# Kernel optimization log

Measured on AMD Instinct MI355X. Metric: run time of the kernel, lower is better.

Reference implementation:

```python
import jax, jax.numpy as jnp
import numpy as np

HEADS, DH, RS = 8, 32, 16  # heads, dim_head, reduce_size

def _dwconv(x, w):
    # depthwise 3x3, pad=1, stride=1 (OIHW with I=1, groups=C)
    return jax.lax.conv_general_dilated(x, w, (1, 1), [(1, 1), (1, 1)],
        dimension_numbers=('NCHW', 'OIHW', 'NCHW'), feature_group_count=x.shape[1])

def _pwconv(x, w):
    return jax.lax.conv_general_dilated(x, w, (1, 1), 'VALID',
        dimension_numbers=('NCHW', 'OIHW', 'NCHW'))

def _bilinear_ac(x, oh, ow):
    # F.interpolate(mode='bilinear', align_corners=True)
    B, C, H, W = x.shape
    ys = jnp.linspace(0., H - 1., oh)
    xs = jnp.linspace(0., W - 1., ow)
    y0 = jnp.floor(ys).astype(jnp.int32); y1 = jnp.minimum(y0 + 1, H - 1)
    x0 = jnp.floor(xs).astype(jnp.int32); x1 = jnp.minimum(x0 + 1, W - 1)
    wy = (ys - y0)[None, None, :, None]
    wx = (xs - x0)[None, None, None, :]
    top = x[:, :, y0, :] * (1. - wy) + x[:, :, y1, :] * wy
    return top[:, :, :, x0] * (1. - wx) + top[:, :, :, x1] * wx

def _ln(t, g, b, eps=1e-6):
    # per-head LayerNorm over last dim; g,b: [heads, dim_head]
    mu = t.mean(-1, keepdims=True)
    var = ((t - mu) ** 2).mean(-1, keepdims=True)
    return (t - mu) / jnp.sqrt(var + eps) * g[None, :, None, :] + b[None, :, None, :]

def setup_inputs() -> dict:
    key = jax.random.key(0)
    ks = jax.random.split(key, 6)
    C = HEADS * DH  # 256
    x = jax.random.normal(ks[0], (8, C, 64, 64), jnp.float32)
    qkv_dw = jax.random.normal(ks[1], (C, 1, 3, 3), jnp.float32) * 0.05
    qkv_pw = jax.random.normal(ks[2], (3 * C, C, 1, 1), jnp.float32) * 0.05
    out_dw = jax.random.normal(ks[3], (C, 1, 3, 3), jnp.float32) * 0.05
    out_pw = jax.random.normal(ks[4], (C, C, 1, 1), jnp.float32) * 0.05
    gq = jnp.ones((HEADS, DH), jnp.float32); bq = jnp.zeros((HEADS, DH), jnp.float32)
    gk = jnp.ones((HEADS, DH), jnp.float32); bk = jnp.zeros((HEADS, DH), jnp.float32)
    bias_table = jax.random.normal(ks[5], ((2 * RS - 1) * (2 * RS - 1), HEADS), jnp.float32) * 0.02
    # relative_position_index buffer, exactly as in RelativePositionBias.__init__
    coords = np.stack(np.meshgrid(np.arange(RS), np.arange(RS), indexing='ij')).reshape(2, -1)
    rel = (coords[:, :, None] - coords[:, None, :]).transpose(1, 2, 0).copy()
    rel[:, :, 0] += RS - 1; rel[:, :, 1] += RS - 1; rel[:, :, 0] *= 2 * RS - 1
    rel_index = jnp.asarray(rel.sum(-1), jnp.int32)  # [RS*RS, RS*RS]
    return dict(x=x, qkv_dw=qkv_dw, qkv_pw=qkv_pw, out_dw=out_dw, out_pw=out_pw,
                gq=gq, bq=bq, gk=gk, bk=bk, bias_table=bias_table, rel_index=rel_index)

def reference(x, qkv_dw, qkv_pw, out_dw, out_pw, gq, bq, gk, bk, bias_table, rel_index):
    B, C, H, W = x.shape
    qkv = _pwconv(_dwconv(x, qkv_dw), qkv_pw)          # [B, 3*inner_dim, H, W]
    q, k, v = jnp.split(qkv, 3, axis=1)
    k = _bilinear_ac(k, RS, RS)
    v = _bilinear_ac(v, RS, RS)
    def heads(t):  # 'b (dim_head heads) h w -> b heads (h w) dim_head'
        b, _, hh, ww = t.shape
        return t.reshape(b, DH, HEADS, hh * ww).transpose(0, 2, 3, 1)
    q = _ln(heads(q), gq, bq)                           # [B, h, H*W, DH]
    k = _ln(heads(k), gk, bk)                           # [B, h, RS*RS, DH]
    v = heads(v)
    attn = jnp.einsum('bhid,bhjd->bhij', q, k)          # [B, h, H*W, RS*RS]
    # relative position bias: gather + repeat_interleave expansion
    bias = bias_table[rel_index.reshape(-1)].reshape(RS, RS, RS * RS, HEADS)
    bias = jnp.repeat(jnp.repeat(bias, H // RS, axis=0), W // RS, axis=1)
    bias = bias.reshape(H * W, RS * RS, HEADS).transpose(2, 0, 1)[None]
    attn = (attn + bias) * (1.0 / DH)                   # scale = dim_head ** -1 (no softmax)
    out = jnp.einsum('bhij,bhjd->bhid', attn, v)        # [B, h, H*W, DH]
    out = out.reshape(B, HEADS, H, W, DH).transpose(0, 4, 1, 2, 3).reshape(B, DH * HEADS, H, W)
    out = _pwconv(_dwconv(out, out_dw), out_pw)
    return out, attn
```

## Files before the change

### kernel.cpp

```cpp
#include <hip/hip_runtime.h>
#include <cstdint>

#define HW_ 4096

typedef __attribute__((ext_vector_type(8))) short bf16x8;
typedef __attribute__((ext_vector_type(4))) short bf16x4;
typedef __attribute__((ext_vector_type(4))) float f32x4;

static __device__ __forceinline__ unsigned short f2bf(float f) {
  unsigned u = __builtin_bit_cast(unsigned, f);
  u += 0x7FFF + ((u >> 16) & 1);
  return (unsigned short)(u >> 16);
}
static __device__ __forceinline__ float bf2f(unsigned short u) {
  return __builtin_bit_cast(float, (unsigned)u << 16);
}
static __device__ __forceinline__ float ldf(const float* p) { return *p; }
static __device__ __forceinline__ float ldf(const unsigned short* p) { return bf2f(*p); }

static __device__ __forceinline__ void gl_lds16(const unsigned short* g,
                                                unsigned short* s) {
  __builtin_amdgcn_global_load_lds(
      (const __attribute__((address_space(1))) unsigned int*)g,
      (__attribute__((address_space(3))) unsigned int*)s, 16, 0, 0);
}

template <typename T, int DO_PREP>
__global__ __launch_bounds__(256) void dwconv_t_kernel(
    const T* __restrict__ x, const float* __restrict__ w9,
    unsigned short* __restrict__ xT,
    const float* __restrict__ pw1, const float* __restrict__ pw2,
    unsigned short* __restrict__ wb, const float* __restrict__ btab,
    const int* __restrict__ relidx, float* __restrict__ bias_pre) {
  if (DO_PREP && blockIdx.z == 8) {
    int idx0 = (blockIdx.y * 64 + blockIdx.x) * 256 + threadIdx.x;
#pragma unroll
    for (int k = 0; k < 12; ++k) {
      int idx = idx0 + k * 65536;
      if (idx < 262144) {
        wb[idx] = f2bf(idx < 196608 ? pw1[idx] : pw2[idx - 196608]);
      } else {
        int t = idx - 262144;
        int j = t & 255, g = (t >> 8) & 255, h = t >> 16;
        bias_pre[t] = btab[relidx[g * 256 + j] * 8 + h] * 0.03125f;
      }
    }
    return;
  }
  __shared__ unsigned short lds_t[64][66];
  int iy = blockIdx.x;
  int cg = blockIdx.y;
  int b  = blockIdx.z;
  int tid = threadIdx.x;
  int px  = tid & 63;
  int cl0 = (tid >> 6) * 16;
  const T* xrow = x + (size_t)b * 256 * HW_ + iy * 64 + px;
#pragma unroll 4
  for (int e = 0; e < 16; ++e) {
    int c = cg * 64 + cl0 + e;
    const T* xp = xrow + (size_t)c * HW_;
    const float* wp = w9 + c * 9;
    float v0 = (iy > 0)  ? ldf(xp - 64) : 0.f;
    float v1 = ldf(xp);
    float v2 = (iy < 63) ? ldf(xp + 64) : 0.f;
    float l0 = __shfl(v0, px - 1, 64), r0 = __shfl(v0, px + 1, 64);
    float l1 = __shfl(v1, px - 1, 64), r1 = __shfl(v1, px + 1, 64);
    float l2 = __shfl(v2, px - 1, 64), r2 = __shfl(v2, px + 1, 64);
    if (px == 0)  { l0 = 0.f; l1 = 0.f; l2 = 0.f; }
    if (px == 63) { r0 = 0.f; r1 = 0.f; r2 = 0.f; }
    float acc = l0 * wp[0] + v0 * wp[1] + r0 * wp[2]
              + l1 * wp[3] + v1 * wp[4] + r1 * wp[5]
              + l2 * wp[6] + v2 * wp[7] + r2 * wp[8];
    lds_t[cl0 + e][px] = f2bf(acc);
  }
  __syncthreads();
#pragma unroll
  for (int j = 0; j < 2; ++j) {
    int flat = tid + j * 256;
    int rpx = flat >> 3, cseg = flat & 7;
    unsigned v0 = (unsigned)lds_t[cseg*8+0][rpx] | ((unsigned)lds_t[cseg*8+1][rpx] << 16);
    unsigned v1 = (unsigned)lds_t[cseg*8+2][rpx] | ((unsigned)lds_t[cseg*8+3][rpx] << 16);
    unsigned v2 = (unsigned)lds_t[cseg*8+4][rpx] | ((unsigned)lds_t[cseg*8+5][rpx] << 16);
    unsigned v3 = (unsigned)lds_t[cseg*8+6][rpx] | ((unsigned)lds_t[cseg*8+7][rpx] << 16);
    uint4 pk = {v0, v1, v2, v3};
    *(uint4*)(xT + ((size_t)b * 4096 + iy * 64 + rpx) * 256 + cg * 64 + cseg * 8) = pk;
  }
}

template <int OUT_BF16, int KV>
__global__ __launch_bounds__(256) void pwconv_mfma_kernel(
    const unsigned short* __restrict__ XT, const unsigned short* __restrict__ W,
    void* __restrict__ Yv, int OC,
    const float* __restrict__ gk, const float* __restrict__ bk,
    unsigned short* __restrict__ kln, unsigned short* __restrict__ vfrag) {
  __shared__ unsigned short As[128 * 64];
  __shared__ unsigned short Bs[128 * 64];
  int tid = threadIdx.x;
  int b = blockIdx.z;
  if (KV && blockIdx.y == 2) {
    float (*xds)[260] = (float(*)[260])As;
    int j0 = blockIdx.x * 8;
    {
      int pt = tid >> 5, icg = tid & 31;
      int j = j0 + pt;
      int oy = j >> 4, ox = j & 15;
      const float s = 63.0f / 15.0f;
      float ys = oy * s, xf = ox * s;
      int y0 = (int)ys, x0 = (int)xf;
      int y1 = min(y0 + 1, 63), x1 = min(x0 + 1, 63);
      float wy = ys - (float)y0, wx = xf - (float)x0;
      float w00 = (1.f - wy) * (1.f - wx), w01 = (1.f - wy) * wx;
      float w10 = wy * (1.f - wx), w11 = wy * wx;
      const unsigned short* base = XT + (size_t)b * 4096 * 256 + icg * 8;
      bf16x8 a00 = *(const bf16x8*)(base + (size_t)(y0 * 64 + x0) * 256);
      bf16x8 a01 = *(const bf16x8*)(base + (size_t)(y0 * 64 + x1) * 256);
      bf16x8 a10 = *(const bf16x8*)(base + (size_t)(y1 * 64 + x0) * 256);
      bf16x8 a11 = *(const bf16x8*)(base + (size_t)(y1 * 64 + x1) * 256);
#pragma unroll
      for (int e = 0; e < 8; ++e) {
        xds[pt][icg * 8 + e] =
            w00 * bf2f((unsigned short)a00[e]) + w01 * bf2f((unsigned short)a01[e]) +
            w10 * bf2f((unsigned short)a10[e]) + w11 * bf2f((unsigned short)a11[e]);
      }
    }
    __syncthreads();
    int pt = tid & 7, grp = tid >> 3;
    int isv = grp >> 4, h = (grp >> 1) & 7, dh = grp & 1;
    int j = j0 + pt;
    int bh = b * 8 + h;
    float acc[16] = {};
    const unsigned short* Wb = W + (size_t)(256 + isv * 256 + dh * 128 + h) * 256;
    for (int c8 = 0; c8 < 32; ++c8) {
      const float4* xr = (const float4*)&xds[pt][c8 * 8];
      float4 xa = xr[0], xb = xr[1];
#pragma unroll
      for (int dd = 0; dd < 16; ++dd) {
        bf16x8 wv = *(const bf16x8*)(Wb + (size_t)dd * 8 * 256 + c8 * 8);
        acc[dd] += bf2f((unsigned short)wv[0]) * xa.x + bf2f((unsigned short)wv[1]) * xa.y
                 + bf2f((unsigned short)wv[2]) * xa.z + bf2f((unsigned short)wv[3]) * xa.w
                 + bf2f((unsigned short)wv[4]) * xb.x + bf2f((unsigned short)wv[5]) * xb.y
                 + bf2f((unsigned short)wv[6]) * xb.z + bf2f((unsigned short)wv[7]) * xb.w;
      }
    }
    if (isv == 0) {
      float s1 = 0.f, s2 = 0.f;
#pragma unroll
      for (int dd = 0; dd < 16; ++dd) { s1 += acc[dd]; s2 += acc[dd] * acc[dd]; }
      s1 += __shfl_xor(s1, 8, 64);
      s2 += __shfl_xor(s2, 8, 64);
      float mu = s1 * (1.f / 32.f);
      float var = s2 * (1.f / 32.f) - mu * mu;
      float inv = 1.0f / sqrtf(var + 1e-6f);
      unsigned r[8];
#pragma unroll
      for (int t = 0; t < 8; ++t) {
        int d = dh * 16 + 2 * t;
        float y0f = (acc[2*t]   - mu) * inv * gk[h*32 + d]     + bk[h*32 + d];
        float y1f = (acc[2*t+1] - mu) * inv * gk[h*32 + d + 1] + bk[h*32 + d + 1];
        r[t] = (unsigned)f2bf(y0f) | ((unsigned)f2bf(y1f) << 16);
      }
      unsigned short* ko = kln + ((size_t)bh * 256 + j) * 32 + dh * 16;
      uint4 p0 = {r[0], r[1], r[2], r[3]};
      uint4 p1 = {r[4], r[5], r[6], r[7]};
      *(uint4*)ko = p0;
      *(uint4*)(ko + 8) = p1;
    } else {
      int c = j >> 4, gq2 = (j >> 2) & 3, ii = j & 3;
      unsigned short* vo = vfrag + (size_t)bh * 32 * 256 + (c * 2 + dh) * 256 + ii;
#pragma unroll
      for (int dd = 0; dd < 16; ++dd)
        vo[(gq2 * 16 + dd) * 4] = f2bf(acc[dd]);
    }
    return;
  }
  int oc0 = blockIdx.y * 128, p0 = blockIdx.x * 128;
  int w = tid >> 6, l = tid & 63;
  int wm = w >> 1, wn = w & 1;
  int lr = l & 15, lg = l >> 4;
  const unsigned short* Wp = W + (size_t)oc0 * 256;
  const unsigned short* Xp = XT + ((size_t)b * 4096 + p0) * 256;
  f32x4 acc[4][4] = {};
  for (int kt = 0; kt < 4; ++kt) {
    int k0 = kt * 64;
#pragma unroll
    for (int j = 0; j < 4; ++j) {
      int chunk = w * 4 + j;
      int row = chunk * 8 + (l >> 3);
      int lcu = (l & 7) ^ (row & 7);
      gl_lds16(Wp + (size_t)row * 256 + k0 + lcu * 8, &As[chunk * 512]);
      gl_lds16(Xp + (size_t)row * 256 + k0 + lcu * 8, &Bs[chunk * 512]);
    }
    __syncthreads();
#pragma unroll
    for (int ks = 0; ks < 2; ++ks) {
      bf16x8 af[4], bfr[4];
      int ku = ks * 4 + lg;
#pragma unroll
      for (int mi = 0; mi < 4; ++mi) {
        int row = wm * 64 + mi * 16 + lr;
        af[mi] = *(const bf16x8*)&As[row * 64 + (ku ^ (row & 7)) * 8];
      }
#pragma unroll
      for (int ni = 0; ni < 4; ++ni) {
        int row = wn * 64 + ni * 16 + lr;
        bfr[ni] = *(const bf16x8*)&Bs[row * 64 + (ku ^ (row & 7)) * 8];
      }
#pragma unroll
      for (int mi = 0; mi < 4; ++mi)
#pragma unroll
        for (int ni = 0; ni < 4; ++ni)
          acc[mi][ni] = __builtin_amdgcn_mfma_f32_16x16x32_bf16(
              af[mi], bfr[ni], acc[mi][ni], 0, 0, 0);
    }
    __syncthreads();
  }
  if constexpr (OUT_BF16) {
    __shared__ unsigned short Cs[128][136];
#pragma unroll
    for (int mi = 0; mi < 4; ++mi)
#pragma unroll
      for (int ni = 0; ni < 4; ++ni)
#pragma unroll
        for (int r = 0; r < 4; ++r)
          Cs[wm * 64 + mi * 16 + lg * 4 + r][wn * 64 + ni * 16 + lr] =
              f2bf(acc[mi][ni][r]);
    __syncthreads();
    unsigned short* Yb = (unsigned short*)Yv + (size_t)b * OC * HW_;
    int pc = tid & 15, ocr = tid >> 4;
#pragma unroll
    for (int it = 0; it < 8; ++it) {
      int oc = it * 16 + ocr;
      uint4 pk = *(const uint4*)&Cs[oc][pc * 8];
      *(uint4*)(Yb + (size_t)(oc0 + oc) * HW_ + p0 + pc * 8) = pk;
    }
  } else {
    float* Yb = (float*)Yv + (size_t)b * OC * HW_;
#pragma unroll
    for (int mi = 0; mi < 4; ++mi)
#pragma unroll
      for (int ni = 0; ni < 4; ++ni)
#pragma unroll
        for (int r = 0; r < 4; ++r) {
          int oc = oc0 + wm * 64 + mi * 16 + lg * 4 + r;
          int p  = p0 + wn * 64 + ni * 16 + lr;
          Yb[(size_t)oc * HW_ + p] = acc[mi][ni][r];
        }
  }
}

__global__ __launch_bounds__(256) void attn_mfma_kernel(
    const unsigned short* __restrict__ qb, const float* __restrict__ gq,
    const float* __restrict__ bq, const unsigned short* __restrict__ kln,
    const unsigned short* __restrict__ vfrag, const float* __restrict__ bias_pre,
    float* __restrict__ attn_out, unsigned short* __restrict__ out_nchw) {
  int tile = blockIdx.x, h = blockIdx.y, b = blockIdx.z;
  int bh = b * 8 + h;
  int tid = threadIdx.x;
  int w = tid >> 6, l = tid & 63;
  int lr = l & 15, lg = l >> 4;
  int qbase = tile * 64 + w * 16;
  int q = qbase + lr;
  int iy = q >> 6, ix = q & 63;
  int g = (iy >> 2) * 16 + (ix >> 2);

  const unsigned short* qp = qb + ((size_t)b * 256 + h) * HW_ + q;
  float qv[8];
  float sum = 0.f, sum2 = 0.f;
#pragma unroll
  for (int e = 0; e < 8; ++e) {
    qv[e] = bf2f(qp[(size_t)((lg * 8 + e) * 8) * HW_]);
    sum += qv[e]; sum2 += qv[e] * qv[e];
  }
  sum  += __shfl_xor(sum, 16, 64);  sum  += __shfl_xor(sum, 32, 64);
  sum2 += __shfl_xor(sum2, 16, 64); sum2 += __shfl_xor(sum2, 32, 64);
  float mu = sum * (1.f / 32.f);
  float var = sum2 * (1.f / 32.f) - mu * mu;
  float inv = 1.0f / sqrtf(var + 1e-6f);
  bf16x8 qf;
#pragma unroll
  for (int e = 0; e < 8; ++e) {
    int d = lg * 8 + e;
    float y = (qv[e] - mu) * inv * gq[h * 32 + d] + bq[h * 32 + d];
    qf[e] = (short)f2bf(y);
  }

  const unsigned short* kbase = kln + (size_t)bh * 256 * 32 + lr * 32 + lg * 8;
  const unsigned short* vbase = vfrag + (size_t)bh * 32 * 256 + l * 4;
  const float* bbase = bias_pre + ((size_t)h * 256 + g) * 256 + lg * 4;
  float* abase = attn_out + ((size_t)bh * 4096 + q) * 256 + lg * 4;

  f32x4 z = {0.f, 0.f, 0.f, 0.f};
  f32x4 oacc0 = z, oacc1 = z;
#pragma unroll
  for (int c = 0; c < 16; ++c) {
    bf16x8 kf = *(const bf16x8*)(kbase + c * 16 * 32);
    f32x4 s = __builtin_amdgcn_mfma_f32_16x16x32_bf16(kf, qf, z, 0, 0, 0);
    f32x4 bias = *(const f32x4*)(bbase + c * 16);
    f32x4 t = s * 0.03125f + bias;
    __builtin_nontemporal_store(t, (f32x4*)(abase + c * 16));
    bf16x4 pb;
    pb[0] = (short)f2bf(t.x);
    pb[1] = (short)f2bf(t.y);
    pb[2] = (short)f2bf(t.z);
    pb[3] = (short)f2bf(t.w);
    bf16x4 va0 = *(const bf16x4*)(vbase + (c * 2 + 0) * 256);
    bf16x4 va1 = *(const bf16x4*)(vbase + (c * 2 + 1) * 256);
    oacc0 = __builtin_amdgcn_mfma_f32_16x16x16bf16_1k(va0, pb, oacc0, 0, 0, 0);
    oacc1 = __builtin_amdgcn_mfma_f32_16x16x16bf16_1k(va1, pb, oacc1, 0, 0, 0);
  }
  float ov[8] = {oacc0.x, oacc0.y, oacc0.z, oacc0.w,
                 oacc1.x, oacc1.y, oacc1.z, oacc1.w};
#pragma unroll
  for (int dt = 0; dt < 2; ++dt) {
#pragma unroll
    for (int r = 0; r < 4; ++r) {
      int d = dt * 16 + lg * 4 + r;
      int cc = d * 8 + h;
      out_nchw[((size_t)b * 256 + cc) * HW_ + qbase + lr] = f2bf(ov[dt * 4 + r]);
    }
  }
}

extern "C" void kernel_launch(void* const* d_in, const int* in_sizes, int n_in,
                              void* d_out, int out_size, void* d_ws, size_t ws_size,
                              hipStream_t stream) {
  const float* x      = (const float*)d_in[0];
  const float* qkv_dw = (const float*)d_in[1];
  const float* qkv_pw = (const float*)d_in[2];
  const float* out_dw = (const float*)d_in[3];
  const float* out_pw = (const float*)d_in[4];
  const float* gq     = (const float*)d_in[5];
  const float* bq     = (const float*)d_in[6];
  const float* gk     = (const float*)d_in[7];
  const float* bk     = (const float*)d_in[8];
  const float* btab   = (const float*)d_in[9];
  const int*   relidx = (const int*)d_in[10];

  float* out  = (float*)d_out;
  float* attn = out + 8388608;

  unsigned short* us = (unsigned short*)d_ws;
  unsigned short* xT1    = us;
  unsigned short* xT2    = us + 8388608;
  unsigned short* onchwb = us + 16777216;
  unsigned short* kln    = us + 25165824;
  unsigned short* vfrag  = us + 25690112;
  unsigned short* wbuf   = us + 26214400;
  float* bias_pre = (float*)(us + 26476544);
  unsigned short* qb     = us + 27525120;

  dwconv_t_kernel<float, 1><<<dim3(64, 4, 9), 256, 0, stream>>>(
      x, qkv_dw, xT1, qkv_pw, out_pw, wbuf, btab, relidx, bias_pre);
  pwconv_mfma_kernel<1, 1><<<dim3(32, 3, 8), 256, 0, stream>>>(
      xT1, wbuf, qb, 256, gk, bk, kln, vfrag);
  attn_mfma_kernel<<<dim3(64, 8, 8), 256, 0, stream>>>(qb, gq, bq, kln, vfrag,
                                                       bias_pre, attn, onchwb);
  dwconv_t_kernel<unsigned short, 0><<<dim3(64, 4, 8), 256, 0, stream>>>(
      onchwb, out_dw, xT2, nullptr, nullptr, nullptr, nullptr, nullptr, nullptr);
  pwconv_mfma_kernel<0, 0><<<dim3(32, 2, 8), 256, 0, stream>>>(
      xT2, wbuf + 196608, out, 256, nullptr, nullptr, nullptr, nullptr);
}
```

Before: 168.6 us.

## Move K/V projection to separate MFMA GEMM kernel with head-permuted weights

The scalar FP32 K/V projection that ran inside the q pwconv kernel is replaced. That kernel now only bilinearly downsamples the input to a bf16 buffer. A new kv_gemm_kernel then does the K/V projection with bf16 MFMA, followed by LayerNorm and the vfrag scatter. The weight prep permutes the K/V weight rows so that each head's channels are contiguous, and the LDS is shared with the epilogue buffer. This trades an extra kernel launch, a global round-trip of the downsampled tensor, and bf16 rounding of the downsampled input for much cheaper matrix math.

```diff
diff --git a/kernel.cpp b/kernel.cpp
--- a/kernel.cpp
+++ b/kernel.cpp
@@ -37,8 +37,20 @@
 #pragma unroll
     for (int k = 0; k < 12; ++k) {
       int idx = idx0 + k * 65536;
-      if (idx < 262144) {
-        wb[idx] = f2bf(idx < 196608 ? pw1[idx] : pw2[idx - 196608]);
+      if (idx < 65536) {
+        wb[idx] = f2bf(pw1[idx]);
+      } else if (idx < 131072) {
+        int t = idx - 65536;
+        int row = t >> 8, col = t & 255;
+        int h = row >> 5, d = row & 31;
+        wb[idx] = f2bf(pw1[(256 + d * 8 + h) * 256 + col]);
+      } else if (idx < 196608) {
+        int t = idx - 131072;
+        int row = t >> 8, col = t & 255;
+        int h = row >> 5, d = row & 31;
+        wb[idx] = f2bf(pw1[(512 + d * 8 + h) * 256 + col]);
+      } else if (idx < 262144) {
+        wb[idx] = f2bf(pw2[idx - 196608]);
       } else {
         int t = idx - 262144;
         int j = t & 255, g = (t >> 8) & 255, h = t >> 16;
@@ -90,86 +102,45 @@
 template <int OUT_BF16, int KV>
 __global__ __launch_bounds__(256) void pwconv_mfma_kernel(
     const unsigned short* __restrict__ XT, const unsigned short* __restrict__ W,
-    void* __restrict__ Yv, int OC,
-    const float* __restrict__ gk, const float* __restrict__ bk,
-    unsigned short* __restrict__ kln, unsigned short* __restrict__ vfrag) {
-  __shared__ unsigned short As[128 * 64];
-  __shared__ unsigned short Bs[128 * 64];
+    void* __restrict__ Yv, int OC, unsigned short* __restrict__ xds) {
+  __shared__ unsigned short smem[18432];
+  unsigned short* As = smem;
+  unsigned short* Bs = smem + 8192;
   int tid = threadIdx.x;
   int b = blockIdx.z;
   if (KV && blockIdx.y == 2) {
-    float (*xds)[260] = (float(*)[260])As;
-    int j0 = blockIdx.x * 8;
-    {
-      int pt = tid >> 5, icg = tid & 31;
-      int j = j0 + pt;
-      int oy = j >> 4, ox = j & 15;
-      const float s = 63.0f / 15.0f;
-      float ys = oy * s, xf = ox * s;
-      int y0 = (int)ys, x0 = (int)xf;
-      int y1 = min(y0 + 1, 63), x1 = min(x0 + 1, 63);
-      float wy = ys - (float)y0, wx = xf - (float)x0;
-      float w00 = (1.f - wy) * (1.f - wx), w01 = (1.f - wy) * wx;
-      float w10 = wy * (1.f - wx), w11 = wy * wx;
-      const unsigned short* base = XT + (size_t)b * 4096 * 256 + icg * 8;
-      bf16x8 a00 = *(const bf16x8*)(base + (size_t)(y0 * 64 + x0) * 256);
-      bf16x8 a01 = *(const bf16x8*)(base + (size_t)(y0 * 64 + x1) * 256);
-      bf16x8 a10 = *(const bf16x8*)(base + (size_t)(y1 * 64 + x0) * 256);
-      bf16x8 a11 = *(const bf16x8*)(base + (size_t)(y1 * 64 + x1) * 256);
-#pragma unroll
-      for (int e = 0; e < 8; ++e) {
-        xds[pt][icg * 8 + e] =
-            w00 * bf2f((unsigned short)a00[e]) + w01 * bf2f((unsigned short)a01[e]) +
-            w10 * bf2f((unsigned short)a10[e]) + w11 * bf2f((unsigned short)a11[e]);
-      }
-    }
-    __syncthreads();
-    int pt = tid & 7, grp = tid >> 3;
-    int isv = grp >> 4, h = (grp >> 1) & 7, dh = grp & 1;
-    int j = j0 + pt;
-    int bh = b * 8 + h;
-    float acc[16] = {};
-    const unsigned short* Wb = W + (size_t)(256 + isv * 256 + dh * 128 + h) * 256;
-    for (int c8 = 0; c8 < 32; ++c8) {
-      const float4* xr = (const float4*)&xds[pt][c8 * 8];
-      float4 xa = xr[0], xb = xr[1];
-#pragma unroll
-      for (int dd = 0; dd < 16; ++dd) {
-        bf16x8 wv = *(const bf16x8*)(Wb + (size_t)dd * 8 * 256 + c8 * 8);
-        acc[dd] += bf2f((unsigned short)wv[0]) * xa.x + bf2f((unsigned short)wv[1]) * xa.y
-                 + bf2f((unsigned short)wv[2]) * xa.z + bf2f((unsigned short)wv[3]) * xa.w
-                 + bf2f((unsigned short)wv[4]) * xb.x + bf2f((unsigned short)wv[5]) * xb.y
-                 + bf2f((unsigned short)wv[6]) * xb.z + bf2f((unsigned short)wv[7]) * xb.w;
-      }
-    }
-    if (isv == 0) {
-      float s1 = 0.f, s2 = 0.f;
-#pragma unroll
-      for (int dd = 0; dd < 16; ++dd) { s1 += acc[dd]; s2 += acc[dd] * acc[dd]; }
-      s1 += __shfl_xor(s1, 8, 64);
-      s2 += __shfl_xor(s2, 8, 64);
-      float mu = s1 * (1.f / 32.f);
-      float var = s2 * (1.f / 32.f) - mu * mu;
-      float inv = 1.0f / sqrtf(var + 1e-6f);
-      unsigned r[8];
-#pragma unroll
-      for (int t = 0; t < 8; ++t) {
-        int d = dh * 16 + 2 * t;
-        float y0f = (acc[2*t]   - mu) * inv * gk[h*32 + d]     + bk[h*32 + d];
-        float y1f = (acc[2*t+1] - mu) * inv * gk[h*32 + d + 1] + bk[h*32 + d + 1];
-        r[t] = (unsigned)f2bf(y0f) | ((unsigned)f2bf(y1f) << 16);
-      }
-      unsigned short* ko = kln + ((size_t)bh * 256 + j) * 32 + dh * 16;
-      uint4 p0 = {r[0], r[1], r[2], r[3]};
-      uint4 p1 = {r[4], r[5], r[6], r[7]};
-      *(uint4*)ko = p0;
-      *(uint4*)(ko + 8) = p1;
-    } else {
-      int c = j >> 4, gq2 = (j >> 2) & 3, ii = j & 3;
-      unsigned short* vo = vfrag + (size_t)bh * 32 * 256 + (c * 2 + dh) * 256 + ii;
-#pragma unroll
-      for (int dd = 0; dd < 16; ++dd)
-        vo[(gq2 * 16 + dd) * 4] = f2bf(acc[dd]);
+    if (blockIdx.x >= 8) return;
+    int j0 = blockIdx.x * 32;
+    int jloc = tid >> 3, icg = tid & 7;
+    int j = j0 + jloc;
+    int oy = j >> 4, ox = j & 15;
+    const float s = 63.0f / 15.0f;
+    float ys = oy * s, xf = ox * s;
+    int y0 = (int)ys, x0 = (int)xf;
+    int y1 = min(y0 + 1, 63), x1 = min(x0 + 1, 63);
+    float wy = ys - (float)y0, wx = xf - (float)x0;
+    float w00 = (1.f - wy) * (1.f - wx), w01 = (1.f - wy) * wx;
+    float w10 = wy * (1.f - wx), w11 = wy * wx;
+    const unsigned short* base = XT + (size_t)b * 4096 * 256 + icg * 32;
+    const bf16x8* p00 = (const bf16x8*)(base + (size_t)(y0 * 64 + x0) * 256);
+    const bf16x8* p01 = (const bf16x8*)(base + (size_t)(y0 * 64 + x1) * 256);
+    const bf16x8* p10 = (const bf16x8*)(base + (size_t)(y1 * 64 + x0) * 256);
+    const bf16x8* p11 = (const bf16x8*)(base + (size_t)(y1 * 64 + x1) * 256);
+    unsigned short* xo = xds + ((size_t)(b * 256 + j)) * 256 + icg * 32;
+#pragma unroll
+    for (int q = 0; q < 4; ++q) {
+      bf16x8 a00 = p00[q], a01 = p01[q], a10 = p10[q], a11 = p11[q];
+      unsigned rp[4];
+#pragma unroll
+      for (int e2 = 0; e2 < 4; ++e2) {
+        float f0 = w00 * bf2f((unsigned short)a00[2*e2])   + w01 * bf2f((unsigned short)a01[2*e2])
+                 + w10 * bf2f((unsigned short)a10[2*e2])   + w11 * bf2f((unsigned short)a11[2*e2]);
+        float f1 = w00 * bf2f((unsigned short)a00[2*e2+1]) + w01 * bf2f((unsigned short)a01[2*e2+1])
+                 + w10 * bf2f((unsigned short)a10[2*e2+1]) + w11 * bf2f((unsigned short)a11[2*e2+1]);
+        rp[e2] = (unsigned)f2bf(f0) | ((unsigned)f2bf(f1) << 16);
+      }
+      uint4 pk = {rp[0], rp[1], rp[2], rp[3]};
+      *(uint4*)(xo + q * 8) = pk;
     }
     return;
   }
@@ -215,7 +186,7 @@
     __syncthreads();
   }
   if constexpr (OUT_BF16) {
-    __shared__ unsigned short Cs[128][136];
+    unsigned short (*Cs)[136] = (unsigned short(*)[136])smem;
 #pragma unroll
     for (int mi = 0; mi < 4; ++mi)
 #pragma unroll
@@ -245,6 +216,117 @@
           int p  = p0 + wn * 64 + ni * 16 + lr;
           Yb[(size_t)oc * HW_ + p] = acc[mi][ni][r];
         }
+  }
+}
+
+__global__ __launch_bounds__(256) void kv_gemm_kernel(
+    const unsigned short* __restrict__ XDS, const unsigned short* __restrict__ W,
+    const float* __restrict__ gk, const float* __restrict__ bk,
+    unsigned short* __restrict__ kln, unsigned short* __restrict__ vfrag) {
+  __shared__ unsigned short smem[18432];
+  unsigned short* As = smem;
+  unsigned short* Bs = smem + 8192;
+  int tid = threadIdx.x;
+  int b = blockIdx.z, yv = blockIdx.y;
+  int oc0 = yv * 128, p0 = blockIdx.x * 128;
+  int w = tid >> 6, l = tid & 63;
+  int wm = w >> 1, wn = w & 1;
+  int lr = l & 15, lg = l >> 4;
+  const unsigned short* Wp = W + (size_t)oc0 * 256;
+  const unsigned short* Xp = XDS + ((size_t)b * 256 + p0) * 256;
+  f32x4 acc[4][4] = {};
+  for (int kt = 0; kt < 4; ++kt) {
+    int k0 = kt * 64;
+#pragma unroll
+    for (int j = 0; j < 4; ++j) {
+      int chunk = w * 4 + j;
+      int row = chunk * 8 + (l >> 3);
+      int lcu = (l & 7) ^ (row & 7);
+      gl_lds16(Wp + (size_t)row * 256 + k0 + lcu * 8, &As[chunk * 512]);
+      gl_lds16(Xp + (size_t)row * 256 + k0 + lcu * 8, &Bs[chunk * 512]);
+    }
+    __syncthreads();
+#pragma unroll
+    for (int ks = 0; ks < 2; ++ks) {
+      bf16x8 af[4], bfr[4];
+      int ku = ks * 4 + lg;
+#pragma unroll
+      for (int mi = 0; mi < 4; ++mi) {
+        int row = wm * 64 + mi * 16 + lr;
+        af[mi] = *(const bf16x8*)&As[row * 64 + (ku ^ (row & 7)) * 8];
+      }
+#pragma unroll
+      for (int ni = 0; ni < 4; ++ni) {
+        int row = wn * 64 + ni * 16 + lr;
+        bfr[ni] = *(const bf16x8*)&Bs[row * 64 + (ku ^ (row & 7)) * 8];
+      }
+#pragma unroll
+      for (int mi = 0; mi < 4; ++mi)
+#pragma unroll
+        for (int ni = 0; ni < 4; ++ni)
+          acc[mi][ni] = __builtin_amdgcn_mfma_f32_16x16x32_bf16(
+              af[mi], bfr[ni], acc[mi][ni], 0, 0, 0);
+    }
+    __syncthreads();
+  }
+  unsigned short (*Cs)[136] = (unsigned short(*)[136])smem;
+#pragma unroll
+  for (int mi = 0; mi < 4; ++mi)
+#pragma unroll
+    for (int ni = 0; ni < 4; ++ni)
+#pragma unroll
+      for (int r = 0; r < 4; ++r)
+        Cs[wm * 64 + mi * 16 + lg * 4 + r][wn * 64 + ni * 16 + lr] =
+            f2bf(acc[mi][ni][r]);
+  __syncthreads();
+  int hl = tid >> 6;
+  int jl = tid & 63;
+  if (yv < 2) {
+    int h = yv * 4 + hl;
+    int bh = b * 8 + h;
+#pragma unroll
+    for (int jj = 0; jj < 2; ++jj) {
+      int jc = jl * 2 + jj;
+      int j = p0 + jc;
+      float v[32];
+      float s1 = 0.f, s2 = 0.f;
+#pragma unroll
+      for (int d = 0; d < 32; ++d) {
+        v[d] = bf2f(Cs[hl * 32 + d][jc]);
+        s1 += v[d]; s2 += v[d] * v[d];
+      }
+      float mu = s1 * (1.f / 32.f);
+      float var = s2 * (1.f / 32.f) - mu * mu;
+      float inv = 1.0f / sqrtf(var + 1e-6f);
+      unsigned rp[16];
+#pragma unroll
+      for (int t = 0; t < 16; ++t) {
+        float y0f = (v[2*t]   - mu) * inv * gk[h*32 + 2*t]   + bk[h*32 + 2*t];
+        float y1f = (v[2*t+1] - mu) * inv * gk[h*32 + 2*t+1] + bk[h*32 + 2*t+1];
+        rp[t] = (unsigned)f2bf(y0f) | ((unsigned)f2bf(y1f) << 16);
+      }
+      uint4* ko = (uint4*)(kln + ((size_t)bh * 256 + j) * 32);
+#pragma unroll
+      for (int t4 = 0; t4 < 4; ++t4) {
+        uint4 pk = {rp[t4*4], rp[t4*4+1], rp[t4*4+2], rp[t4*4+3]};
+        ko[t4] = pk;
+      }
+    }
+  } else {
+    int h = (yv - 2) * 4 + hl;
+    int bh = b * 8 + h;
+#pragma unroll
+    for (int jj = 0; jj < 2; ++jj) {
+      int jc = jl * 2 + jj;
+      int j = p0 + jc;
+      int c = j >> 4, gq2 = (j >> 2) & 3, ii = j & 3;
+      unsigned short* vo = vfrag + (size_t)bh * 8192;
+#pragma unroll
+      for (int d = 0; d < 32; ++d) {
+        int dt = d >> 4, dr = d & 15;
+        vo[(c * 2 + dt) * 256 + (gq2 * 16 + dr) * 4 + ii] = Cs[hl * 32 + d][jc];
+      }
+    }
   }
 }
 
@@ -348,15 +430,18 @@
   unsigned short* wbuf   = us + 26214400;
   float* bias_pre = (float*)(us + 26476544);
   unsigned short* qb     = us + 27525120;
+  unsigned short* xds    = us + 35913728;
 
   dwconv_t_kernel<float, 1><<<dim3(64, 4, 9), 256, 0, stream>>>(
       x, qkv_dw, xT1, qkv_pw, out_pw, wbuf, btab, relidx, bias_pre);
   pwconv_mfma_kernel<1, 1><<<dim3(32, 3, 8), 256, 0, stream>>>(
-      xT1, wbuf, qb, 256, gk, bk, kln, vfrag);
+      xT1, wbuf, qb, 256, xds);
+  kv_gemm_kernel<<<dim3(2, 4, 8), 256, 0, stream>>>(
+      xds, wbuf + 65536, gk, bk, kln, vfrag);
   attn_mfma_kernel<<<dim3(64, 8, 8), 256, 0, stream>>>(qb, gq, bq, kln, vfrag,
                                                        bias_pre, attn, onchwb);
   dwconv_t_kernel<unsigned short, 0><<<dim3(64, 4, 8), 256, 0, stream>>>(
       onchwb, out_dw, xT2, nullptr, nullptr, nullptr, nullptr, nullptr, nullptr);
   pwconv_mfma_kernel<0, 0><<<dim3(32, 2, 8), 256, 0, stream>>>(
-      xT2, wbuf + 196608, out, 256, nullptr, nullptr, nullptr, nullptr);
-}
+      xT2, wbuf + 196608, out, 256, nullptr);
+}
```

Measured after the change: 149.7 us. 11.2% less time.
